# Kernel optimization log

Measured on AMD Instinct MI355X. Metric: run time of the kernel, lower is better.

Reference implementation:

```python
import jax, jax.numpy as jnp
import numpy as np
import math

B, L, D, H = 2, 2048, 1024, 16
HD = D // H  # head dim = 64


def setup_inputs() -> dict:
    key = jax.random.key(0)
    ks = jax.random.split(key, 5)
    s = 0.02
    return {
        "x": jax.random.normal(ks[0], (B, L, D), dtype=jnp.float32),
        "w_qkv": jax.random.normal(ks[1], (D, 3 * D), dtype=jnp.float32) * s,
        "b_qkv": jnp.zeros((3 * D,), dtype=jnp.float32),
        "w_out": jax.random.normal(ks[2], (D, D), dtype=jnp.float32) * s,
        "b_out": jnp.zeros((D,), dtype=jnp.float32),
    }


def reference(x, w_qkv, b_qkv, w_out, b_out):
    Bc, Lc, Dc = x.shape
    qkv = x @ w_qkv + b_qkv  # [B, L, 3D]
    q, k, v = jnp.split(qkv, 3, axis=-1)
    # [B, H, L, hd]
    q = q.reshape(Bc, Lc, H, HD).transpose(0, 2, 1, 3)
    k = k.reshape(Bc, Lc, H, HD).transpose(0, 2, 1, 3)
    v = v.reshape(Bc, Lc, H, HD).transpose(0, 2, 1, 3)
    scores = jnp.einsum("bhqd,bhkd->bhqk", q, k) / math.sqrt(HD)
    causal = jnp.tril(jnp.ones((Lc, Lc), dtype=bool))
    scores = jnp.where(causal[None, None, :, :], scores, -jnp.inf)
    probs = jax.nn.softmax(scores, axis=-1)
    outs = jnp.einsum("bhqk,bhkd->bhqd", probs, v)  # [B, H, L, hd]
    outs = outs.transpose(0, 2, 1, 3).reshape(Bc, Lc, Dc)
    return outs @ w_out + b_out
```

## Files before the change

kernel.cpp:

```cpp
#include <hip/hip_runtime.h>
#include <hip/hip_bf16.h>


using bf16x8 = __attribute__((ext_vector_type(8))) short;
using f32x4  = __attribute__((ext_vector_type(4))) float;

static __device__ __forceinline__ unsigned short f2b(float f) {
  unsigned u = __builtin_bit_cast(unsigned, f);
  unsigned r = (u + 0x7fffu + ((u >> 16) & 1u)) >> 16;
  return (unsigned short)r;
}

static __device__ __forceinline__ unsigned cvtpk(float lo, float hi) {
  unsigned r;
  asm("v_cvt_pk_bf16_f32 %0, %1, %2" : "=v"(r) : "v"(lo), "v"(hi));
  return r;
}

static __device__ __forceinline__ void gl_lds16(const void* g, void* l) {
  __builtin_amdgcn_global_load_lds(
      (const __attribute__((address_space(1))) unsigned int*)g,
      (__attribute__((address_space(3))) unsigned int*)l, 16, 0, 0);
}

__global__ __launch_bounds__(256) void convert_bf16(
    const float* __restrict__ in, unsigned short* __restrict__ out, int n8) {
  int i = blockIdx.x * 256 + threadIdx.x;
  if (i >= n8) return;
  const float4* p = reinterpret_cast<const float4*>(in) + (size_t)i * 2;
  float4 a = p[0], b = p[1];
  bf16x8 o;
  o[0] = f2b(a.x); o[1] = f2b(a.y); o[2] = f2b(a.z); o[3] = f2b(a.w);
  o[4] = f2b(b.x); o[5] = f2b(b.y); o[6] = f2b(b.z); o[7] = f2b(b.w);
  reinterpret_cast<bf16x8*>(out)[i] = o;
}

__global__ __launch_bounds__(256) void transpose_convert(
    const float* __restrict__ w, unsigned short* __restrict__ wt, int K, int N) {
  int idx = blockIdx.x * 256 + threadIdx.x;
  int n  = idx % N;
  int k0 = (idx / N) * 8;
  if (k0 >= K) return;
  bf16x8 o;
#pragma unroll
  for (int j = 0; j < 8; ++j) o[j] = f2b(w[(size_t)(k0 + j) * N + n]);
  *reinterpret_cast<bf16x8*>(&wt[(size_t)n * K + k0]) = o;
}

__global__ __launch_bounds__(256) void transpose_v(
    const unsigned short* __restrict__ vb, unsigned short* __restrict__ vt) {
  __shared__ unsigned short T[64][72];
  const int bh = blockIdx.y, l0 = blockIdx.x * 64;
  const int row = threadIdx.x >> 2;
  const int qc  = threadIdx.x & 3;
#pragma unroll
  for (int h = 0; h < 2; ++h) {
    bf16x8 v = *reinterpret_cast<const bf16x8*>(
        &vb[((size_t)bh * 2048 + l0 + row) * 64 + h * 32 + qc * 8]);
#pragma unroll
    for (int j = 0; j < 8; ++j) T[h * 32 + qc * 8 + j][row] = (unsigned short)v[j];
  }
  __syncthreads();
#pragma unroll
  for (int h = 0; h < 2; ++h) {
    bf16x8 o = *reinterpret_cast<const bf16x8*>(&T[row][h * 32 + qc * 8]);
    *reinterpret_cast<bf16x8*>(
        &vt[((size_t)bh * 64 + row) * 2048 + l0 + h * 32 + qc * 8]) = o;
  }
}

__global__ __launch_bounds__(512) void gemm_qkv(
    const unsigned short* __restrict__ A,
    const unsigned short* __restrict__ Bt,
    const float* __restrict__ bias,
    unsigned short* __restrict__ qb, unsigned short* __restrict__ kb,
    unsigned short* __restrict__ vb) {
  __shared__ __align__(16) unsigned short lA[256 * 64];
  __shared__ __align__(16) unsigned short lB[128 * 64];
  const int t = threadIdx.x;
  const int lin = blockIdx.y * 24 + blockIdx.x;
  const int nb  = (lin & 7) * 48 + (lin >> 3);
  const int bm = nb / 24, bn = nb % 24;
  const int s0 = (nb * 5) & 15;
  const int w = t >> 6, lane = t & 63;
  const int lr = lane & 15, lg = lane >> 4;
  const int wm = (w >> 1) * 64, wn = (w & 1) * 64;
  const int g8  = lane >> 3;
  const int swz = ((lane & 7) * 16) ^ (g8 << 4);

  f32x4 acc[4][4];
#pragma unroll
  for (int i = 0; i < 4; ++i)
#pragma unroll
    for (int j = 0; j < 4; ++j) acc[i][j] = f32x4{0.f, 0.f, 0.f, 0.f};

  const size_t am = (size_t)bm * 256, bnr = (size_t)bn * 128;

  for (int kt = 0; kt < 16; ++kt) {
    const int k0 = ((kt + s0) & 15) * 64;
#pragma unroll
    for (int i = 0; i < 4; ++i) {
      const int rs = i * 64 + w * 8;
      gl_lds16((const char*)(A + (am + rs + g8) * 1024 + k0) + swz,
               (char*)lA + rs * 128);
    }
#pragma unroll
    for (int i = 0; i < 2; ++i) {
      const int rs = i * 64 + w * 8;
      gl_lds16((const char*)(Bt + (bnr + rs + g8) * 1024 + k0) + swz,
               (char*)lB + rs * 128);
    }
    __syncthreads();
#pragma unroll
    for (int kk = 0; kk < 64; kk += 32) {
      bf16x8 af[4], bfr[4];
#pragma unroll
      for (int fm = 0; fm < 4; ++fm) {
        int row = wm + fm * 16 + lr;
        af[fm] = *reinterpret_cast<const bf16x8*>(
            (const char*)lA + row * 128 + ((2 * kk + lg * 16) ^ ((lr & 7) << 4)));
      }
#pragma unroll
      for (int fn = 0; fn < 4; ++fn) {
        int row = wn + fn * 16 + lr;
        bfr[fn] = *reinterpret_cast<const bf16x8*>(
            (const char*)lB + row * 128 + ((2 * kk + lg * 16) ^ ((lr & 7) << 4)));
      }
#pragma unroll
      for (int fm = 0; fm < 4; ++fm)
#pragma unroll
        for (int fn = 0; fn < 4; ++fn)
          acc[fm][fn] = __builtin_amdgcn_mfma_f32_16x16x32_bf16(
              af[fm], bfr[fn], acc[fm][fn], 0, 0, 0);
    }
    __syncthreads();
  }

#pragma unroll
  for (int fm = 0; fm < 4; ++fm) {
#pragma unroll
    for (int fn = 0; fn < 4; ++fn) {
#pragma unroll
      for (int r = 0; r < 4; ++r) {
        int row = bm * 256 + wm + fm * 16 + lg * 4 + r;
        int col = bn * 128 + wn + fn * 16 + lr;
        float v = acc[fm][fn][r] + bias[col];
        int bb = row >> 11, l = row & 2047;
        int which = col >> 10, hn = col & 1023;
        int h = hn >> 6, d = hn & 63;
        int bh = bb * 16 + h;
        if (which == 0)
          qb[((size_t)bh * 2048 + l) * 64 + d] = f2b(v * 0.180336879f);
        else if (which == 1)
          kb[((size_t)bh * 2048 + l) * 64 + d] = f2b(v);
        else
          vb[((size_t)bh * 2048 + l) * 64 + d] = f2b(v);
      }
    }
  }
}

__global__ __launch_bounds__(256) void gemm128(
    const unsigned short* __restrict__ A,
    const unsigned short* __restrict__ Bt,
    const float* __restrict__ bias, float* __restrict__ outf) {
  __shared__ __align__(16) unsigned short lA[128 * 64];
  __shared__ __align__(16) unsigned short lB[128 * 64];
  const int t = threadIdx.x;
  const int lin = blockIdx.y * 8 + blockIdx.x;
  const int nb  = (lin & 7) * 32 + (lin >> 3);
  const int bm = nb >> 3, bn = nb & 7;
  const int s0 = (nb * 5) & 15;
  const int w = t >> 6, lane = t & 63;
  const int lr = lane & 15, lg = lane >> 4;
  const int wm = (w >> 1) * 64, wn = (w & 1) * 64;
  const int g8  = lane >> 3;
  const int swz = ((lane & 7) * 16) ^ (g8 << 4);

  f32x4 acc[4][4];
#pragma unroll
  for (int i = 0; i < 4; ++i)
#pragma unroll
    for (int j = 0; j < 4; ++j) acc[i][j] = f32x4{0.f, 0.f, 0.f, 0.f};

  const size_t am = (size_t)bm * 128, bnr = (size_t)bn * 128;

  for (int kt = 0; kt < 16; ++kt) {
    const int k0 = ((kt + s0) & 15) * 64;
#pragma unroll
    for (int i = 0; i < 4; ++i) {
      const int rs = i * 32 + w * 8;
      gl_lds16((const char*)(A + (am + rs + g8) * 1024 + k0) + swz,
               (char*)lA + rs * 128);
      gl_lds16((const char*)(Bt + (bnr + rs + g8) * 1024 + k0) + swz,
               (char*)lB + rs * 128);
    }
    __syncthreads();
#pragma unroll
    for (int kk = 0; kk < 64; kk += 32) {
      bf16x8 af[4], bfr[4];
#pragma unroll
      for (int fm = 0; fm < 4; ++fm) {
        int row = wm + fm * 16 + lr;
        af[fm] = *reinterpret_cast<const bf16x8*>(
            (const char*)lA + row * 128 + ((2 * kk + lg * 16) ^ ((lr & 7) << 4)));
      }
#pragma unroll
      for (int fn = 0; fn < 4; ++fn) {
        int row = wn + fn * 16 + lr;
        bfr[fn] = *reinterpret_cast<const bf16x8*>(
            (const char*)lB + row * 128 + ((2 * kk + lg * 16) ^ ((lr & 7) << 4)));
      }
#pragma unroll
      for (int fm = 0; fm < 4; ++fm)
#pragma unroll
        for (int fn = 0; fn < 4; ++fn)
          acc[fm][fn] = __builtin_amdgcn_mfma_f32_16x16x32_bf16(
              af[fm], bfr[fn], acc[fm][fn], 0, 0, 0);
    }
    __syncthreads();
  }

#pragma unroll
  for (int fm = 0; fm < 4; ++fm)
#pragma unroll
    for (int fn = 0; fn < 4; ++fn)
#pragma unroll
      for (int r = 0; r < 4; ++r) {
        int row = bm * 128 + wm + fm * 16 + lg * 4 + r;
        int col = bn * 128 + wn + fn * 16 + lr;
        outf[(size_t)row * 1024 + col] = acc[fm][fn][r] + bias[col];
      }
}

__global__ __launch_bounds__(256, 2) void attn_kernel(
    const unsigned short* __restrict__ qb, const unsigned short* __restrict__ kb,
    const unsigned short* __restrict__ vt, unsigned short* __restrict__ attnb) {
  __shared__ __align__(16) unsigned short lK[2][128 * 64];
  __shared__ __align__(16) unsigned short lV[2][2][64 * 64];
  __shared__ __align__(16) unsigned short pl[4][16 * 128];
  const int bid = blockIdx.x;
  const int xcd = bid & 7, pos = bid >> 3;
  const int half = pos >> 5, idx = pos & 31;
  const int bh = xcd * 4 + half * 2 + (idx >> 4);
  const int qt = half ? (15 - (idx & 15)) : (idx & 15);
  const int q0 = qt * 128;
  const int w = threadIdx.x >> 6, lane = threadIdx.x & 63;
  const int lr = lane & 15, lg = lane >> 4;
  const int g8  = lane >> 3;
  const int swz = ((lane & 7) * 16) ^ (g8 << 4);

  const unsigned short* Kg = kb + (size_t)bh * 2048 * 64;
  const unsigned short* Vg = vt + (size_t)bh * 64 * 2048;

  auto stage = [&](int buf, int c) {
    const size_t kv0 = (size_t)c * 128;
#pragma unroll
    for (int i = 0; i < 4; ++i) {
      const int rs = i * 32 + w * 8;
      gl_lds16((const char*)(Kg + (kv0 + rs + g8) * 64) + swz,
               (char*)&lK[buf][0] + rs * 128);
    }
#pragma unroll
    for (int h = 0; h < 2; ++h)
#pragma unroll
      for (int i = 0; i < 2; ++i) {
        const int rs = i * 32 + w * 8;
        gl_lds16((const char*)(Vg + (size_t)(rs + g8) * 2048 + kv0 + h * 64) + swz,
                 (char*)&lV[buf][h][0] + rs * 128);
      }
  };

  bf16x8 qf[2][2];
#pragma unroll
  for (int qi = 0; qi < 2; ++qi)
#pragma unroll
    for (int kk = 0; kk < 2; ++kk)
      qf[qi][kk] = *reinterpret_cast<const bf16x8*>(
          &qb[((size_t)bh * 2048 + q0 + w * 32 + qi * 16 + lr) * 64 + kk * 32 + lg * 8]);

  f32x4 acc[2][4];
#pragma unroll
  for (int qi = 0; qi < 2; ++qi)
#pragma unroll
    for (int i = 0; i < 4; ++i) acc[qi][i] = f32x4{0.f, 0.f, 0.f, 0.f};
  float m[2] = {-1e30f, -1e30f}, rs[2] = {0.f, 0.f};

  const int nc = qt + 1;
  stage(0, 0);

  for (int c = 0; c < nc; ++c) {
    const int cur = c & 1;
    __syncthreads();
    if (c + 1 < nc) stage(cur ^ 1, c + 1);

    f32x4 s[2][8];
#pragma unroll
    for (int qi = 0; qi < 2; ++qi)
#pragma unroll
      for (int i = 0; i < 8; ++i) s[qi][i] = f32x4{0.f, 0.f, 0.f, 0.f};
#pragma unroll
    for (int nf = 0; nf < 8; ++nf) {
      const int row = nf * 16 + lr;
      bf16x8 k0 = *reinterpret_cast<const bf16x8*>(
          (const char*)&lK[cur][0] + row * 128 + ((lg * 16) ^ ((lr & 7) << 4)));
      bf16x8 k1 = *reinterpret_cast<const bf16x8*>(
          (const char*)&lK[cur][0] + row * 128 + ((64 + lg * 16) ^ ((lr & 7) << 4)));
#pragma unroll
      for (int qi = 0; qi < 2; ++qi) {
        s[qi][nf] = __builtin_amdgcn_mfma_f32_16x16x32_bf16(k0, qf[qi][0], s[qi][nf], 0, 0, 0);
        s[qi][nf] = __builtin_amdgcn_mfma_f32_16x16x32_bf16(k1, qf[qi][1], s[qi][nf], 0, 0, 0);
      }
    }

#pragma unroll
    for (int qi = 0; qi < 2; ++qi) {
      const int qrow = q0 + w * 32 + qi * 16 + lr;
      const bool diag = (c * 128 + 127) > (q0 + w * 32 + qi * 16);
      float ps[8][4];
      float mx = -1e30f;
      if (diag) {
#pragma unroll
        for (int nf = 0; nf < 8; ++nf)
#pragma unroll
          for (int r = 0; r < 4; ++r) {
            int key = c * 128 + nf * 16 + lg * 4 + r;
            float sv = (key <= qrow) ? s[qi][nf][r] : -1e30f;
            ps[nf][r] = sv;
            mx = fmaxf(mx, sv);
          }
      } else {
#pragma unroll
        for (int nf = 0; nf < 8; ++nf)
#pragma unroll
          for (int r = 0; r < 4; ++r) {
            ps[nf][r] = s[qi][nf][r];
            mx = fmaxf(mx, ps[nf][r]);
          }
      }
      mx = fmaxf(mx, __shfl_xor(mx, 16));
      mx = fmaxf(mx, __shfl_xor(mx, 32));
      if (__any(mx > m[qi] + 8.f)) {
        float mn = fmaxf(m[qi], mx);
        float scl = exp2f(m[qi] - mn);
        m[qi] = mn;
        rs[qi] *= scl;
#pragma unroll
        for (int df = 0; df < 4; ++df) acc[qi][df] *= scl;
      }
      float ss = 0.f;
#pragma unroll
      for (int nf = 0; nf < 8; ++nf)
#pragma unroll
        for (int r = 0; r < 4; ++r) {
          float pe = exp2f(ps[nf][r] - m[qi]);
          ps[nf][r] = pe;
          ss += pe;
        }
      ss += __shfl_xor(ss, 16);
      ss += __shfl_xor(ss, 32);
      rs[qi] += ss;

#pragma unroll
      for (int nf = 0; nf < 8; ++nf) {
        uint2 pk;
        pk.x = cvtpk(ps[nf][0], ps[nf][1]);
        pk.y = cvtpk(ps[nf][2], ps[nf][3]);
        *reinterpret_cast<uint2*>(
            (char*)&pl[w][0] + lr * 256 + ((nf * 32 + lg * 8) ^ ((lr & 7) << 4))) = pk;
      }
#pragma unroll
      for (int kk = 0; kk < 4; ++kk) {
        bf16x8 pf = *reinterpret_cast<const bf16x8*>(
            (const char*)&pl[w][0] + lr * 256 + ((kk * 64 + lg * 16) ^ ((lr & 7) << 4)));
#pragma unroll
        for (int df = 0; df < 4; ++df) {
          const int row = df * 16 + lr;
          bf16x8 vf = *reinterpret_cast<const bf16x8*>(
              (const char*)&lV[cur][kk >> 1][0] + row * 128 +
              (((kk & 1) * 64 + lg * 16) ^ ((lr & 7) << 4)));
          acc[qi][df] = __builtin_amdgcn_mfma_f32_16x16x32_bf16(vf, pf, acc[qi][df], 0, 0, 0);
        }
      }
    }
  }

  const int b = bh >> 4, h = bh & 15;
#pragma unroll
  for (int qi = 0; qi < 2; ++qi) {
    float inv = 1.f / rs[qi];
    int qrow = q0 + w * 32 + qi * 16 + lr;
#pragma unroll
    for (int df = 0; df < 4; ++df) {
      ushort4 ov;
      ov.x = f2b(acc[qi][df][0] * inv); ov.y = f2b(acc[qi][df][1] * inv);
      ov.z = f2b(acc[qi][df][2] * inv); ov.w = f2b(acc[qi][df][3] * inv);
      *reinterpret_cast<ushort4*>(
          &attnb[((size_t)b * 2048 + qrow) * 1024 + h * 64 + df * 16 + lg * 4]) = ov;
    }
  }
}

extern "C" void kernel_launch(void* const* d_in, const int* in_sizes, int n_in,
                              void* d_out, int out_size, void* d_ws, size_t ws_size,
                              hipStream_t stream) {
  const float* x     = (const float*)d_in[0];
  const float* w_qkv = (const float*)d_in[1];
  const float* b_qkv = (const float*)d_in[2];
  const float* w_out = (const float*)d_in[3];
  const float* b_out = (const float*)d_in[4];
  float* out = (float*)d_out;
  char* ws = (char*)d_ws;

  unsigned short* xb    = (unsigned short*)(ws);
  unsigned short* vt    = (unsigned short*)(ws);
  unsigned short* wqkvt = (unsigned short*)(ws + 8388608);
  unsigned short* woutt = (unsigned short*)(ws + 14680064);
  unsigned short* qb    = (unsigned short*)(ws + 16777216);
  unsigned short* kb    = (unsigned short*)(ws + 25165824);
  unsigned short* vb    = (unsigned short*)(ws + 33554432);
  unsigned short* attnb = (unsigned short*)(ws + 41943040);

  convert_bf16<<<2048, 256, 0, stream>>>(x, xb, 4194304 / 8);
  transpose_convert<<<1536, 256, 0, stream>>>(w_qkv, wqkvt, 1024, 3072);
  transpose_convert<<<512, 256, 0, stream>>>(w_out, woutt, 1024, 1024);
  gemm_qkv<<<dim3(24, 16), 512, 0, stream>>>(xb, wqkvt, b_qkv, qb, kb, vb);
  transpose_v<<<dim3(32, 32), 256, 0, stream>>>(vb, vt);
  attn_kernel<<<512, 256, 0, stream>>>(qb, kb, vt, attnb);
  gemm128<<<dim3(8, 32), 256, 0, stream>>>(attnb, woutt, b_out, out);
}
```

Baseline: 135.2 us.

## Switch attention to 32x32x16 MFMA and keep P in registers via lane shuffles

The attention kernel moves from 16x16x32 to 32x32x16 bf16 MFMA tiles, so each wave handles all 32 of its query rows as one MFMA column block. The softmax probabilities are reordered between lane halves with __shfl_xor and fed straight into the PV MFMA, which removes the per-wave LDS scratch buffer and its write/read round trip. The row max and sum reductions need one shuffle instead of two. The cost is more registers per thread for the 16-wide accumulators (sf[4] and acc[2]), which could cut occupancy under the 256-thread, 2-block launch bound.

```diff
diff --git a/kernel.cpp b/kernel.cpp
--- a/kernel.cpp
+++ b/kernel.cpp
@@ -4,6 +4,7 @@
 
 using bf16x8 = __attribute__((ext_vector_type(8))) short;
 using f32x4  = __attribute__((ext_vector_type(4))) float;
+using f32x16 = __attribute__((ext_vector_type(16))) float;
 
 static __device__ __forceinline__ unsigned short f2b(float f) {
   unsigned u = __builtin_bit_cast(unsigned, f);
@@ -238,7 +239,6 @@
     const unsigned short* __restrict__ vt, unsigned short* __restrict__ attnb) {
   __shared__ __align__(16) unsigned short lK[2][128 * 64];
   __shared__ __align__(16) unsigned short lV[2][2][64 * 64];
-  __shared__ __align__(16) unsigned short pl[4][16 * 128];
   const int bid = blockIdx.x;
   const int xcd = bid & 7, pos = bid >> 3;
   const int half = pos >> 5, idx = pos & 31;
@@ -246,7 +246,7 @@
   const int qt = half ? (15 - (idx & 15)) : (idx & 15);
   const int q0 = qt * 128;
   const int w = threadIdx.x >> 6, lane = threadIdx.x & 63;
-  const int lr = lane & 15, lg = lane >> 4;
+  const int l31 = lane & 31, hi = lane >> 5;
   const int g8  = lane >> 3;
   const int swz = ((lane & 7) * 16) ^ (g8 << 4);
 
@@ -271,20 +271,19 @@
       }
   };
 
-  bf16x8 qf[2][2];
-#pragma unroll
-  for (int qi = 0; qi < 2; ++qi)
-#pragma unroll
-    for (int kk = 0; kk < 2; ++kk)
-      qf[qi][kk] = *reinterpret_cast<const bf16x8*>(
-          &qb[((size_t)bh * 2048 + q0 + w * 32 + qi * 16 + lr) * 64 + kk * 32 + lg * 8]);
-
-  f32x4 acc[2][4];
-#pragma unroll
-  for (int qi = 0; qi < 2; ++qi)
-#pragma unroll
-    for (int i = 0; i < 4; ++i) acc[qi][i] = f32x4{0.f, 0.f, 0.f, 0.f};
-  float m[2] = {-1e30f, -1e30f}, rs[2] = {0.f, 0.f};
+  const int qrow = q0 + w * 32 + l31;
+  bf16x8 qf[4];
+#pragma unroll
+  for (int s = 0; s < 4; ++s)
+    qf[s] = *reinterpret_cast<const bf16x8*>(
+        &qb[((size_t)bh * 2048 + qrow) * 64 + s * 16 + hi * 8]);
+
+  f32x16 acc[2];
+#pragma unroll
+  for (int dg = 0; dg < 2; ++dg)
+#pragma unroll
+    for (int r = 0; r < 16; ++r) acc[dg][r] = 0.f;
+  float m = -1e30f, rsum = 0.f;
 
   const int nc = qt + 1;
   stage(0, 0);
@@ -294,111 +293,102 @@
     __syncthreads();
     if (c + 1 < nc) stage(cur ^ 1, c + 1);
 
-    f32x4 s[2][8];
-#pragma unroll
-    for (int qi = 0; qi < 2; ++qi)
-#pragma unroll
-      for (int i = 0; i < 8; ++i) s[qi][i] = f32x4{0.f, 0.f, 0.f, 0.f};
-#pragma unroll
-    for (int nf = 0; nf < 8; ++nf) {
-      const int row = nf * 16 + lr;
-      bf16x8 k0 = *reinterpret_cast<const bf16x8*>(
-          (const char*)&lK[cur][0] + row * 128 + ((lg * 16) ^ ((lr & 7) << 4)));
-      bf16x8 k1 = *reinterpret_cast<const bf16x8*>(
-          (const char*)&lK[cur][0] + row * 128 + ((64 + lg * 16) ^ ((lr & 7) << 4)));
-#pragma unroll
-      for (int qi = 0; qi < 2; ++qi) {
-        s[qi][nf] = __builtin_amdgcn_mfma_f32_16x16x32_bf16(k0, qf[qi][0], s[qi][nf], 0, 0, 0);
-        s[qi][nf] = __builtin_amdgcn_mfma_f32_16x16x32_bf16(k1, qf[qi][1], s[qi][nf], 0, 0, 0);
-      }
-    }
-
-#pragma unroll
-    for (int qi = 0; qi < 2; ++qi) {
-      const int qrow = q0 + w * 32 + qi * 16 + lr;
-      const bool diag = (c * 128 + 127) > (q0 + w * 32 + qi * 16);
-      float ps[8][4];
-      float mx = -1e30f;
-      if (diag) {
-#pragma unroll
-        for (int nf = 0; nf < 8; ++nf)
-#pragma unroll
-          for (int r = 0; r < 4; ++r) {
-            int key = c * 128 + nf * 16 + lg * 4 + r;
-            float sv = (key <= qrow) ? s[qi][nf][r] : -1e30f;
-            ps[nf][r] = sv;
-            mx = fmaxf(mx, sv);
-          }
-      } else {
-#pragma unroll
-        for (int nf = 0; nf < 8; ++nf)
-#pragma unroll
-          for (int r = 0; r < 4; ++r) {
-            ps[nf][r] = s[qi][nf][r];
-            mx = fmaxf(mx, ps[nf][r]);
-          }
-      }
-      mx = fmaxf(mx, __shfl_xor(mx, 16));
-      mx = fmaxf(mx, __shfl_xor(mx, 32));
-      if (__any(mx > m[qi] + 8.f)) {
-        float mn = fmaxf(m[qi], mx);
-        float scl = exp2f(m[qi] - mn);
-        m[qi] = mn;
-        rs[qi] *= scl;
-#pragma unroll
-        for (int df = 0; df < 4; ++df) acc[qi][df] *= scl;
-      }
-      float ss = 0.f;
-#pragma unroll
-      for (int nf = 0; nf < 8; ++nf)
-#pragma unroll
-        for (int r = 0; r < 4; ++r) {
-          float pe = exp2f(ps[nf][r] - m[qi]);
-          ps[nf][r] = pe;
-          ss += pe;
+    f32x16 sf[4];
+#pragma unroll
+    for (int g = 0; g < 4; ++g)
+#pragma unroll
+      for (int r = 0; r < 16; ++r) sf[g][r] = 0.f;
+#pragma unroll
+    for (int st = 0; st < 4; ++st)
+#pragma unroll
+      for (int g = 0; g < 4; ++g) {
+        const int row = g * 32 + l31;
+        bf16x8 kf = *reinterpret_cast<const bf16x8*>(
+            (const char*)&lK[cur][0] + row * 128 +
+            ((st * 32 + hi * 16) ^ ((row & 7) << 4)));
+        sf[g] = __builtin_amdgcn_mfma_f32_32x32x16_bf16(kf, qf[st], sf[g], 0, 0, 0);
+      }
+
+    const bool diag = (c * 128 + 127) > (q0 + w * 32);
+    float mx = -1e30f;
+#pragma unroll
+    for (int g = 0; g < 4; ++g)
+#pragma unroll
+      for (int r = 0; r < 16; ++r) {
+        float sv = sf[g][r];
+        if (diag) {
+          int key = c * 128 + g * 32 + (r & 3) + 8 * (r >> 2) + 4 * hi;
+          sv = (key <= qrow) ? sv : -1e30f;
+          sf[g][r] = sv;
         }
-      ss += __shfl_xor(ss, 16);
-      ss += __shfl_xor(ss, 32);
-      rs[qi] += ss;
-
-#pragma unroll
-      for (int nf = 0; nf < 8; ++nf) {
-        uint2 pk;
-        pk.x = cvtpk(ps[nf][0], ps[nf][1]);
-        pk.y = cvtpk(ps[nf][2], ps[nf][3]);
-        *reinterpret_cast<uint2*>(
-            (char*)&pl[w][0] + lr * 256 + ((nf * 32 + lg * 8) ^ ((lr & 7) << 4))) = pk;
-      }
-#pragma unroll
-      for (int kk = 0; kk < 4; ++kk) {
-        bf16x8 pf = *reinterpret_cast<const bf16x8*>(
-            (const char*)&pl[w][0] + lr * 256 + ((kk * 64 + lg * 16) ^ ((lr & 7) << 4)));
-#pragma unroll
-        for (int df = 0; df < 4; ++df) {
-          const int row = df * 16 + lr;
+        mx = fmaxf(mx, sv);
+      }
+    mx = fmaxf(mx, __shfl_xor(mx, 32));
+    if (__any(mx > m + 8.f)) {
+      float mn = fmaxf(m, mx);
+      float scl = exp2f(m - mn);
+      m = mn;
+      rsum *= scl;
+#pragma unroll
+      for (int dg = 0; dg < 2; ++dg)
+#pragma unroll
+        for (int r = 0; r < 16; ++r) acc[dg][r] *= scl;
+    }
+    float ss = 0.f;
+#pragma unroll
+    for (int g = 0; g < 4; ++g)
+#pragma unroll
+      for (int r = 0; r < 16; ++r) {
+        float pe = exp2f(sf[g][r] - m);
+        sf[g][r] = pe;
+        ss += pe;
+      }
+    ss += __shfl_xor(ss, 32);
+    rsum += ss;
+
+#pragma unroll
+    for (int g = 0; g < 4; ++g) {
+      unsigned dw[8], X[8];
+#pragma unroll
+      for (int tp = 0; tp < 8; ++tp)
+        dw[tp] = cvtpk(sf[g][2 * tp], sf[g][2 * tp + 1]);
+#pragma unroll
+      for (int tp = 0; tp < 8; ++tp) X[tp] = __shfl_xor(dw[tp], 32);
+#pragma unroll
+      for (int st2 = 0; st2 < 2; ++st2) {
+        const int b0 = st2 * 4;
+        uint4 u;
+        u.x = hi ? X[b0 + 2] : dw[b0 + 0];
+        u.y = hi ? X[b0 + 3] : dw[b0 + 1];
+        u.z = hi ? dw[b0 + 2] : X[b0 + 0];
+        u.w = hi ? dw[b0 + 3] : X[b0 + 1];
+        bf16x8 pf = __builtin_bit_cast(bf16x8, u);
+#pragma unroll
+        for (int dg = 0; dg < 2; ++dg) {
+          const int vrow = dg * 32 + l31;
           bf16x8 vf = *reinterpret_cast<const bf16x8*>(
-              (const char*)&lV[cur][kk >> 1][0] + row * 128 +
-              (((kk & 1) * 64 + lg * 16) ^ ((lr & 7) << 4)));
-          acc[qi][df] = __builtin_amdgcn_mfma_f32_16x16x32_bf16(vf, pf, acc[qi][df], 0, 0, 0);
+              (const char*)&lV[cur][g >> 1][0] + vrow * 128 +
+              ((((g & 1) * 64 + st2 * 32 + hi * 16)) ^ ((vrow & 7) << 4)));
+          acc[dg] = __builtin_amdgcn_mfma_f32_32x32x16_bf16(vf, pf, acc[dg], 0, 0, 0);
         }
       }
     }
   }
 
   const int b = bh >> 4, h = bh & 15;
-#pragma unroll
-  for (int qi = 0; qi < 2; ++qi) {
-    float inv = 1.f / rs[qi];
-    int qrow = q0 + w * 32 + qi * 16 + lr;
-#pragma unroll
-    for (int df = 0; df < 4; ++df) {
+  const float inv = 1.f / rsum;
+#pragma unroll
+  for (int dg = 0; dg < 2; ++dg)
+#pragma unroll
+    for (int tq = 0; tq < 4; ++tq) {
       ushort4 ov;
-      ov.x = f2b(acc[qi][df][0] * inv); ov.y = f2b(acc[qi][df][1] * inv);
-      ov.z = f2b(acc[qi][df][2] * inv); ov.w = f2b(acc[qi][df][3] * inv);
+      ov.x = f2b(acc[dg][4 * tq + 0] * inv);
+      ov.y = f2b(acc[dg][4 * tq + 1] * inv);
+      ov.z = f2b(acc[dg][4 * tq + 2] * inv);
+      ov.w = f2b(acc[dg][4 * tq + 3] * inv);
       *reinterpret_cast<ushort4*>(
-          &attnb[((size_t)b * 2048 + qrow) * 1024 + h * 64 + df * 16 + lg * 4]) = ov;
-    }
-  }
+          &attnb[((size_t)b * 2048 + qrow) * 1024 + h * 64 + dg * 32 + 8 * tq + 4 * hi]) = ov;
+    }
 }
 
 extern "C" void kernel_launch(void* const* d_in, const int* in_sizes, int n_in,
```

New measurement: 139.1 us. 1.03x slower.

## Split attention KV loop into two independent softmax streams merged at end

Applied to the files above, without the earlier changes.

The causal attention loop now alternates KV chunks between two independent online-softmax states (separate max, row-sum and output accumulators), unrolled by two. The states are merged in the epilogue with rescaling. The aim is to break the serial dependency on the running max and accumulator between consecutive chunks, so the compiler can interleave MFMA and softmax work across chunks. It doubles accumulator register use, which may lower occupancy or cause spills, and the manual unroll grows code size.

```diff
diff --git a/kernel.cpp b/kernel.cpp
--- a/kernel.cpp
+++ b/kernel.cpp
@@ -279,21 +279,19 @@
       qf[qi][kk] = *reinterpret_cast<const bf16x8*>(
           &qb[((size_t)bh * 2048 + q0 + w * 32 + qi * 16 + lr) * 64 + kk * 32 + lg * 8]);
 
-  f32x4 acc[2][4];
+  f32x4 accA[2][4], accB[2][4];
 #pragma unroll
   for (int qi = 0; qi < 2; ++qi)
 #pragma unroll
-    for (int i = 0; i < 4; ++i) acc[qi][i] = f32x4{0.f, 0.f, 0.f, 0.f};
-  float m[2] = {-1e30f, -1e30f}, rs[2] = {0.f, 0.f};
-
-  const int nc = qt + 1;
-  stage(0, 0);
-
-  for (int c = 0; c < nc; ++c) {
-    const int cur = c & 1;
-    __syncthreads();
-    if (c + 1 < nc) stage(cur ^ 1, c + 1);
-
+    for (int i = 0; i < 4; ++i) {
+      accA[qi][i] = f32x4{0.f, 0.f, 0.f, 0.f};
+      accB[qi][i] = f32x4{0.f, 0.f, 0.f, 0.f};
+    }
+  float mA[2] = {-1e30f, -1e30f}, rsA[2] = {0.f, 0.f};
+  float mB[2] = {-1e30f, -1e30f}, rsB[2] = {0.f, 0.f};
+
+  auto process = [&](int c, int buf, float (&m)[2], float (&rs)[2],
+                     f32x4 (&acc)[2][4]) {
     f32x4 s[2][8];
 #pragma unroll
     for (int qi = 0; qi < 2; ++qi)
@@ -303,9 +301,9 @@
     for (int nf = 0; nf < 8; ++nf) {
       const int row = nf * 16 + lr;
       bf16x8 k0 = *reinterpret_cast<const bf16x8*>(
-          (const char*)&lK[cur][0] + row * 128 + ((lg * 16) ^ ((lr & 7) << 4)));
+          (const char*)&lK[buf][0] + row * 128 + ((lg * 16) ^ ((lr & 7) << 4)));
       bf16x8 k1 = *reinterpret_cast<const bf16x8*>(
-          (const char*)&lK[cur][0] + row * 128 + ((64 + lg * 16) ^ ((lr & 7) << 4)));
+          (const char*)&lK[buf][0] + row * 128 + ((64 + lg * 16) ^ ((lr & 7) << 4)));
 #pragma unroll
       for (int qi = 0; qi < 2; ++qi) {
         s[qi][nf] = __builtin_amdgcn_mfma_f32_16x16x32_bf16(k0, qf[qi][0], s[qi][nf], 0, 0, 0);
@@ -377,24 +375,42 @@
         for (int df = 0; df < 4; ++df) {
           const int row = df * 16 + lr;
           bf16x8 vf = *reinterpret_cast<const bf16x8*>(
-              (const char*)&lV[cur][kk >> 1][0] + row * 128 +
+              (const char*)&lV[buf][kk >> 1][0] + row * 128 +
               (((kk & 1) * 64 + lg * 16) ^ ((lr & 7) << 4)));
           acc[qi][df] = __builtin_amdgcn_mfma_f32_16x16x32_bf16(vf, pf, acc[qi][df], 0, 0, 0);
         }
       }
     }
+  };
+
+  const int nc = qt + 1;
+  stage(0, 0);
+
+  for (int c = 0; c < nc; c += 2) {
+    __syncthreads();
+    if (c + 1 < nc) stage(1, c + 1);
+    process(c, 0, mA, rsA, accA);
+    if (c + 1 < nc) {
+      __syncthreads();
+      if (c + 2 < nc) stage(0, c + 2);
+      process(c + 1, 1, mB, rsB, accB);
+    }
   }
 
   const int b = bh >> 4, h = bh & 15;
 #pragma unroll
   for (int qi = 0; qi < 2; ++qi) {
-    float inv = 1.f / rs[qi];
+    float mm = fmaxf(mA[qi], mB[qi]);
+    float sA = exp2f(mA[qi] - mm), sB = exp2f(mB[qi] - mm);
+    float inv = 1.f / (rsA[qi] * sA + rsB[qi] * sB);
     int qrow = q0 + w * 32 + qi * 16 + lr;
 #pragma unroll
     for (int df = 0; df < 4; ++df) {
       ushort4 ov;
-      ov.x = f2b(acc[qi][df][0] * inv); ov.y = f2b(acc[qi][df][1] * inv);
-      ov.z = f2b(acc[qi][df][2] * inv); ov.w = f2b(acc[qi][df][3] * inv);
+      ov.x = f2b((accA[qi][df][0] * sA + accB[qi][df][0] * sB) * inv);
+      ov.y = f2b((accA[qi][df][1] * sA + accB[qi][df][1] * sB) * inv);
+      ov.z = f2b((accA[qi][df][2] * sA + accB[qi][df][2] * sB) * inv);
+      ov.w = f2b((accA[qi][df][3] * sA + accB[qi][df][3] * sB) * inv);
       *reinterpret_cast<ushort4*>(
           &attnb[((size_t)b * 2048 + qrow) * 1024 + h * 64 + df * 16 + lg * 4]) = ov;
     }
```

After: 148.8 us. 10.1% more time.
